# Optimization experiments

Measured on AMD Instinct MI355X. Metric: run time of the kernel, lower is better.

## Reference

```python
import jax, jax.numpy as jnp
import numpy as np

N_NODES = 50000
N_EDGES = 800000
HID = 64
N_LAYERS = 4
POS_DIM = 3
PARAM_SCALE = 0.1
POS_HEAD_SCALE = 0.001  # xavier gain=0.001 on final pos Linear


def setup_inputs() -> dict:
    key = jax.random.key(0)
    ks = jax.random.split(key, 12)
    L, H = N_LAYERS, HID
    s = PARAM_SCALE
    return {
        "x": jax.random.normal(ks[0], (N_NODES, HID), jnp.float32),
        "pos": jax.random.normal(ks[1], (N_NODES, POS_DIM), jnp.float32),
        "edge_index": jax.random.randint(ks[2], (2, N_EDGES), 0, N_NODES, jnp.int32),
        # edge MLP: Linear(2H+1 -> H), SiLU, Linear(H -> H), SiLU
        "We1": jax.random.normal(ks[3], (L, 2 * H + 1, H), jnp.float32) * s,
        "be1": jnp.zeros((L, H), jnp.float32),
        "We2": jax.random.normal(ks[4], (L, H, H), jnp.float32) * s,
        "be2": jnp.zeros((L, H), jnp.float32),
        # node MLP: Linear(2H -> H), SiLU, Linear(H -> H)
        "Wn1": jax.random.normal(ks[5], (L, 2 * H, H), jnp.float32) * s,
        "bn1": jnp.zeros((L, H), jnp.float32),
        "Wn2": jax.random.normal(ks[6], (L, H, H), jnp.float32) * s,
        "bn2": jnp.zeros((L, H), jnp.float32),
        # pos MLP: Linear(H -> H), SiLU, Linear(H -> 1) (tiny init)
        "Wp1": jax.random.normal(ks[7], (L, H, H), jnp.float32) * s,
        "bp1": jnp.zeros((L, H), jnp.float32),
        "Wp2": jax.random.normal(ks[8], (L, H, 1), jnp.float32) * POS_HEAD_SCALE,
        "bp2": jnp.zeros((L, 1), jnp.float32),
        # logit(pos_scale=0.5) == 0
        "pos_scale_logit": jnp.zeros((1,), jnp.float32),
    }


def reference(x, pos, edge_index, We1, be1, We2, be2, Wn1, bn1, Wn2, bn2,
              Wp1, bp1, Wp2, bp2, pos_scale_logit):
    POS_CLAMP = 500.0
    POS_UPDATE_CLAMP = 5.0
    src, dst = edge_index[0], edge_index[1]  # messages flow j=src -> i=dst
    n = x.shape[0]
    L = We1.shape[0]

    # pos is NOT fed back between layers in the torch forward, so edge
    # geometry is constant across layers.
    rel = pos[dst] - pos[src]                     # [E, P]
    d2 = jnp.sum(rel * rel, axis=-1, keepdims=True)  # [E, 1]
    deg = jnp.maximum(
        jax.ops.segment_sum(jnp.ones(src.shape, x.dtype), dst, num_segments=n),
        1.0)[:, None]                             # [N, 1]

    pos_new = pos
    for l in range(L):
        # edge MLP on gathered node pairs
        m = jnp.concatenate([x[dst], x[src], d2], axis=-1)  # [E, 2H+1]
        m = jax.nn.silu(m @ We1[l] + be1[l])
        m = jax.nn.silu(m @ We2[l] + be2[l])                # [E, H]
        # scatter-aggregate messages to target nodes
        agg = jax.ops.segment_sum(m, dst, num_segments=n)   # [N, H]
        # node update MLP
        h = jax.nn.silu(jnp.concatenate([x, agg], axis=-1) @ Wn1[l] + bn1[l])
        x = h @ Wn2[l] + bn2[l]
        # position update: mean over incoming edges of rel * phi_pos(m)
        c = jax.nn.silu(m @ Wp1[l] + bp1[l]) @ Wp2[l] + bp2[l]  # [E, 1]
        pos_new = pos + jax.ops.segment_sum(rel * c, dst, num_segments=n) / deg

    upd = (pos_new - pos) * jax.nn.sigmoid(pos_scale_logit[0])
    upd = jnp.clip(upd, -POS_UPDATE_CLAMP, POS_UPDATE_CLAMP)
    pos_out = jnp.clip(pos + upd, -POS_CLAMP, POS_CLAMP)
    return x, pos_out
```

## Files before the change

### kernel.cpp

```cpp
#include <hip/hip_runtime.h>

#define NN 50000
#define NE 800000
#define NTILES 12500
#define TPB 17

typedef __attribute__((ext_vector_type(8))) short short8;
typedef __attribute__((ext_vector_type(4))) float f32x4;

__device__ __forceinline__ float silu_f(float v) {
    return v / (1.0f + __expf(-v));
}
__device__ __forceinline__ unsigned short f2bf(float f) {
    unsigned u = __float_as_uint(f);
    u += 0x7fffu + ((u >> 16) & 1u);
    return (unsigned short)(u >> 16);
}
__device__ __forceinline__ unsigned pk2(float a, float b) {
    return (unsigned)f2bf(a) | ((unsigned)f2bf(b) << 16);
}
__device__ __forceinline__ void gload_lds16(const unsigned short* g, unsigned short* l) {
    __builtin_amdgcn_global_load_lds(
        (const __attribute__((address_space(1))) unsigned int*)g,
        (__attribute__((address_space(3))) unsigned int*)l, 16, 0, 0);
}
#define FENCE_BAR() do { \
    asm volatile("s_waitcnt lgkmcnt(0)" ::: "memory"); \
    __builtin_amdgcn_sched_barrier(0); \
    __builtin_amdgcn_s_barrier(); \
    __builtin_amdgcn_sched_barrier(0); \
} while (0)
#define VMDRAIN() do { \
    __builtin_amdgcn_sched_barrier(0); \
    asm volatile("s_waitcnt vmcnt(0)" ::: "memory"); \
    __builtin_amdgcn_sched_barrier(0); \
} while (0)

__global__ __launch_bounds__(256) void egnn_hist(
    const int* __restrict__ dst, int* __restrict__ hc)
{
    int e = blockIdx.x * 256 + threadIdx.x;
    if (e < NE) atomicAdd(&hc[dst[e]], 1);
}

__global__ __launch_bounds__(1024) void egnn_scan(
    int* __restrict__ hc, int* __restrict__ rowptr)
{
    __shared__ int part[1024];
    const int t = threadIdx.x;
    const int C = (NN + 1023) / 1024;
    const int b0 = t * C;
    int s = 0;
    for (int i = 0; i < C; ++i) {
        int idx = b0 + i;
        if (idx < NN) s += hc[idx];
    }
    part[t] = s;
    __syncthreads();
    for (int off = 1; off < 1024; off <<= 1) {
        int v = (t >= off) ? part[t - off] : 0;
        __syncthreads();
        part[t] += v;
        __syncthreads();
    }
    int run = part[t] - s;
    for (int i = 0; i < C; ++i) {
        int idx = b0 + i;
        if (idx < NN) {
            int v = hc[idx];
            rowptr[idx] = run;
            hc[idx] = run;
            run += v;
        }
    }
    if (t == 1023) rowptr[NN] = part[1023];
}

__global__ __launch_bounds__(256) void egnn_scatter(
    const int* __restrict__ src, const int* __restrict__ dst,
    const float* __restrict__ pos, int* __restrict__ cursor,
    int* __restrict__ eSrc, int* __restrict__ eDst, float* __restrict__ eD2)
{
    int e = blockIdx.x * 256 + threadIdx.x;
    if (e >= NE) return;
    int s = src[e], d = dst[e];
    float rx = pos[3*d+0] - pos[3*s+0];
    float ry = pos[3*d+1] - pos[3*s+1];
    float rz = pos[3*d+2] - pos[3*s+2];
    int p = atomicAdd(&cursor[d], 1);
    eSrc[p] = s;
    eDst[p] = d;
    eD2[p]  = rx*rx + ry*ry + rz*rz;
}

__global__ __launch_bounds__(256) void egnn_prep_w(
    const float* __restrict__ We1, const float* __restrict__ We2,
    unsigned short* __restrict__ Wg1, unsigned short* __restrict__ Wg2)
{
    int i = blockIdx.x * 256 + threadIdx.x;
    if (i < 4 * 64 * 128) {
        int k = i & 127, n = (i >> 7) & 63, l = i >> 13;
        Wg1[(size_t)(l * 64 + n) * 136 + k] = f2bf(We1[((size_t)l * 129 + k) * 64 + n]);
    }
    if (i < 4 * 64 * 64) {
        int h = i & 63, n = (i >> 6) & 63, l = i >> 12;
        Wg2[(size_t)(l * 64 + n) * 72 + h] = f2bf(We2[((size_t)l * 64 + h) * 64 + n]);
    }
}

__global__ __launch_bounds__(256) void egnn_prep_wn(
    const float* __restrict__ Wn1, const float* __restrict__ Wn2,
    unsigned short* __restrict__ Wgn1, unsigned short* __restrict__ Wgn2)
{
    int i = blockIdx.x * 256 + threadIdx.x;
    if (i < 4 * 64 * 128) {
        int k = i & 127, n = (i >> 7) & 63, l = i >> 13;
        Wgn1[(size_t)(l * 64 + n) * 136 + k] = f2bf(Wn1[((size_t)l * 128 + k) * 64 + n]);
    }
    if (i < 4 * 64 * 64) {
        int h = i & 63, n = (i >> 6) & 63, l = i >> 12;
        Wgn2[(size_t)(l * 64 + n) * 72 + h] = f2bf(Wn2[((size_t)l * 64 + h) * 64 + n]);
    }
}

__global__ __launch_bounds__(256) void egnn_xbf(
    const float* __restrict__ x, unsigned short* __restrict__ xbf)
{
    int i = blockIdx.x * 256 + threadIdx.x;
    if (i >= NN * 16) return;
    float4 v = ((const float4*)x)[i];
    ((uint2*)xbf)[i] = make_uint2(pk2(v.x, v.y), pk2(v.z, v.w));
}

template<bool POS>
__global__ __launch_bounds__(256) void egnn_edge(
    const unsigned short* __restrict__ xbf, const float* __restrict__ eD2,
    const int* __restrict__ eSrc, const int* __restrict__ eDst,
    const float* __restrict__ pos,
    const unsigned short* __restrict__ Wg1, const unsigned short* __restrict__ Wg2,
    const float* __restrict__ We1,
    const float* __restrict__ be1, const float* __restrict__ be2,
    const float* __restrict__ Wp1, const float* __restrict__ bp1,
    const float* __restrict__ Wp2, const float* __restrict__ bp2,
    float* __restrict__ agg, float* __restrict__ dpos, int layer)
{
    __shared__ __align__(16) unsigned char pool[16384 * 2 + 16640];
    __shared__ int   sS[2][64];
    __shared__ int   sD[2][64];
    __shared__ float s2[2][64];
    __shared__ float sC[64];

    unsigned short* const xls0 = (unsigned short*)pool;
    unsigned short* const xls1 = (unsigned short*)(pool + 16384);
    unsigned short* const m1l  = (unsigned short*)(pool + 32768);
    float* const          sM2f = (float*)(pool + 32768);

    const int t    = threadIdx.x;
    const int lane = t & 63;
    const int w    = t >> 6;
    const int l15  = lane & 15;
    const int g    = lane >> 4;
    const int eh   = w >> 1;
    const int ch   = w & 1;
    const int er   = lane >> 4;
    const int half = (lane >> 3) & 1;
    const int c    = lane & 7;
    const int tile0 = blockIdx.x * TPB;
    const int ntiles = (NTILES - tile0 < TPB) ? (NTILES - tile0) : TPB;

    const unsigned short* W1b = &Wg1[(size_t)(layer * 64) * 136];
    const unsigned short* W2b = &Wg2[(size_t)(layer * 64) * 72];
    short8 w1f0[4], w1f1[4], w2f0[2], w2f1[2];
    #pragma unroll
    for (int ks = 0; ks < 4; ++ks) {
        w1f0[ks] = *(const short8*)&W1b[(ch * 32 +      l15) * 136 + ks * 32 + g * 8];
        w1f1[ks] = *(const short8*)&W1b[(ch * 32 + 16 + l15) * 136 + ks * 32 + g * 8];
    }
    #pragma unroll
    for (int ks = 0; ks < 2; ++ks) {
        w2f0[ks] = *(const short8*)&W2b[(ch * 32 +      l15) * 72 + ks * 32 + g * 8];
        w2f1[ks] = *(const short8*)&W2b[(ch * 32 + 16 + l15) * 72 + ks * 32 + g * 8];
    }
    float4 wrv[2], b1v[2], b2v[2];
    {
        const float* Wr = &We1[((size_t)layer * 129 + 128) * 64];
        const float* B1 = &be1[layer * 64];
        const float* B2 = &be2[layer * 64];
        #pragma unroll
        for (int nt = 0; nt < 2; ++nt) {
            int n0 = ch * 32 + nt * 16 + g * 4;
            wrv[nt] = *(const float4*)&Wr[n0];
            b1v[nt] = *(const float4*)&B1[n0];
            b2v[nt] = *(const float4*)&B2[n0];
        }
    }

    const int* const ip = half ? eSrc : eDst;
    const int ebase = w * 16 + er;

    int nid[4];
    {
        const int gb0 = tile0 * 64;
        #pragma unroll
        for (int i = 0; i < 4; ++i) nid[i] = ip[gb0 + ebase + i * 4];
        #pragma unroll
        for (int i = 0; i < 4; ++i)
            gload_lds16(&xbf[(size_t)nid[i] * 64 + ((c ^ ((ebase + i * 4) & 7)) << 3)],
                        xls0 + w * 2048 + i * 512);
        __builtin_amdgcn_sched_barrier(0);
        if (ntiles > 1) {
            #pragma unroll
            for (int i = 0; i < 4; ++i) nid[i] = ip[gb0 + 64 + ebase + i * 4];
        }
        if (t < 64) { sS[0][t] = eSrc[gb0 + t]; sD[0][t] = eDst[gb0 + t]; s2[0][t] = eD2[gb0 + t]; }
    }
    int stS = 0, stD = 0; float st2 = 0.f;
    if (ntiles > 1 && t < 64) {
        const int gb1 = (tile0 + 1) * 64;
        stS = eSrc[gb1 + t]; stD = eDst[gb1 + t]; st2 = eD2[gb1 + t];
    }
    float bp2v = 0.f;
    if (POS) { bp2v = bp2[layer]; if (t < 64) sC[t] = bp2v; }
    VMDRAIN();
    FENCE_BAR();

    const f32x4 zero = {0.f, 0.f, 0.f, 0.f};

    for (int tt = 0; tt < ntiles; ++tt) {
        const int b = tt & 1;
        unsigned short* const xcur = b ? xls1 : xls0;
        unsigned short* const xnxt = b ? xls0 : xls1;

        if (tt + 1 < ntiles) {
            #pragma unroll
            for (int i = 0; i < 4; ++i)
                gload_lds16(&xbf[(size_t)nid[i] * 64 + ((c ^ ((ebase + i * 4) & 7)) << 3)],
                            xnxt + w * 2048 + i * 512);
            __builtin_amdgcn_sched_barrier(0);
            if (tt + 2 < ntiles) {
                const int gb2 = (tile0 + tt + 2) * 64;
                #pragma unroll
                for (int i = 0; i < 4; ++i) nid[i] = ip[gb2 + ebase + i * 4];
            }
        }

        f32x4 a00 = zero, a01 = zero, a10 = zero, a11 = zero;
        {
            const int r0 = (eh * 32 + l15) * 128;
            const int r1 = r0 + 16 * 128;
            const int r7 = l15 & 7;
            #pragma unroll
            for (int ks = 0; ks < 4; ++ks) {
                int col = (((ks << 2) + g) ^ r7) << 3;
                short8 fb0 = *(const short8*)&xcur[r0 + col];
                short8 fb1 = *(const short8*)&xcur[r1 + col];
                a00 = __builtin_amdgcn_mfma_f32_16x16x32_bf16(w1f0[ks], fb0, a00, 0, 0, 0);
                a01 = __builtin_amdgcn_mfma_f32_16x16x32_bf16(w1f0[ks], fb1, a01, 0, 0, 0);
                a10 = __builtin_amdgcn_mfma_f32_16x16x32_bf16(w1f1[ks], fb0, a10, 0, 0, 0);
                a11 = __builtin_amdgcn_mfma_f32_16x16x32_bf16(w1f1[ks], fb1, a11, 0, 0, 0);
            }
        }
        {
            float d2e0 = s2[b][eh * 32 + l15];
            float d2e1 = s2[b][eh * 32 + 16 + l15];
            int e0 = eh * 32 + l15;
            int e1 = e0 + 16;
            #pragma unroll
            for (int nt = 0; nt < 2; ++nt) {
                int n0 = ch * 32 + nt * 16 + g * 4;
                float4 wr = wrv[nt], bb = b1v[nt];
                f32x4 acc0 = nt ? a10 : a00;
                f32x4 acc1 = nt ? a11 : a01;
                float r0 = silu_f(acc0.x + d2e0 * wr.x + bb.x);
                float r1 = silu_f(acc0.y + d2e0 * wr.y + bb.y);
                float r2 = silu_f(acc0.z + d2e0 * wr.z + bb.z);
                float r3 = silu_f(acc0.w + d2e0 * wr.w + bb.w);
                *(uint2*)&m1l[e0 * 72 + n0] = make_uint2(pk2(r0, r1), pk2(r2, r3));
                r0 = silu_f(acc1.x + d2e1 * wr.x + bb.x);
                r1 = silu_f(acc1.y + d2e1 * wr.y + bb.y);
                r2 = silu_f(acc1.z + d2e1 * wr.z + bb.z);
                r3 = silu_f(acc1.w + d2e1 * wr.w + bb.w);
                *(uint2*)&m1l[e1 * 72 + n0] = make_uint2(pk2(r0, r1), pk2(r2, r3));
            }
        }
        FENCE_BAR();

        f32x4 c00 = zero, c01 = zero, c10 = zero, c11 = zero;
        #pragma unroll
        for (int ks = 0; ks < 2; ++ks) {
            short8 fb0 = *(const short8*)&m1l[(eh * 32 +      l15) * 72 + ks * 32 + g * 8];
            short8 fb1 = *(const short8*)&m1l[(eh * 32 + 16 + l15) * 72 + ks * 32 + g * 8];
            c00 = __builtin_amdgcn_mfma_f32_16x16x32_bf16(w2f0[ks], fb0, c00, 0, 0, 0);
            c01 = __builtin_amdgcn_mfma_f32_16x16x32_bf16(w2f0[ks], fb1, c01, 0, 0, 0);
            c10 = __builtin_amdgcn_mfma_f32_16x16x32_bf16(w2f1[ks], fb0, c10, 0, 0, 0);
            c11 = __builtin_amdgcn_mfma_f32_16x16x32_bf16(w2f1[ks], fb1, c11, 0, 0, 0);
        }
        FENCE_BAR();

        {
            int e0 = eh * 32 + l15;
            int e1 = e0 + 16;
            #pragma unroll
            for (int nt = 0; nt < 2; ++nt) {
                int n0 = ch * 32 + nt * 16 + g * 4;
                float4 bb = b2v[nt];
                f32x4 acc0 = nt ? c10 : c00;
                f32x4 acc1 = nt ? c11 : c01;
                sM2f[e0 * 65 + n0 + 0] = silu_f(acc0.x + bb.x);
                sM2f[e0 * 65 + n0 + 1] = silu_f(acc0.y + bb.y);
                sM2f[e0 * 65 + n0 + 2] = silu_f(acc0.z + bb.z);
                sM2f[e0 * 65 + n0 + 3] = silu_f(acc0.w + bb.w);
                sM2f[e1 * 65 + n0 + 0] = silu_f(acc1.x + bb.x);
                sM2f[e1 * 65 + n0 + 1] = silu_f(acc1.y + bb.y);
                sM2f[e1 * 65 + n0 + 2] = silu_f(acc1.z + bb.z);
                sM2f[e1 * 65 + n0 + 3] = silu_f(acc1.w + bb.w);
            }
        }
        if (tt + 1 < ntiles && t < 64) {
            sS[1 - b][t] = stS; sD[1 - b][t] = stD; s2[1 - b][t] = st2;
            if (tt + 2 < ntiles) {
                const int gb2 = (tile0 + tt + 2) * 64;
                stS = eSrc[gb2 + t]; stD = eDst[gb2 + t]; st2 = eD2[gb2 + t];
            }
        }
        FENCE_BAR();

        if (POS) {
            const int wofs = __builtin_amdgcn_readfirstlane(w * 16);
            float p1[16];
            {
                const float* bP1 = &bp1[(size_t)layer * 64 + wofs];
                #pragma unroll
                for (int hh = 0; hh < 16; ++hh) p1[hh] = bP1[hh];
            }
            const float* P1 = &Wp1[(size_t)layer * 64 * 64 + wofs];
            for (int k = 0; k < 64; ++k) {
                float mv = sM2f[lane * 65 + k];
                const float* wr2 = P1 + k * 64;
                #pragma unroll
                for (int hh = 0; hh < 16; ++hh) p1[hh] = fmaf(mv, wr2[hh], p1[hh]);
            }
            float part = 0.0f;
            {
                const float* P2 = &Wp2[(size_t)layer * 64 + wofs];
                #pragma unroll
                for (int hh = 0; hh < 16; ++hh) part += silu_f(p1[hh]) * P2[hh];
            }
            atomicAdd(&sC[lane], part);
            FENCE_BAR();
            if (w == 0) {
                float cc = sC[lane];
                int d = sD[b][lane], s = sS[b][lane];
                float rx = pos[3*d+0] - pos[3*s+0];
                float ry = pos[3*d+1] - pos[3*s+1];
                float rz = pos[3*d+2] - pos[3*s+2];
                atomicAdd(&dpos[3*(size_t)d+0], rx * cc);
                atomicAdd(&dpos[3*(size_t)d+1], ry * cc);
                atomicAdd(&dpos[3*(size_t)d+2], rz * cc);
            }
            FENCE_BAR();
            if (t < 64) sC[t] = bp2v;
        }

        VMDRAIN();

        {
            const int e0 = w * 16;
            float v[16];
            #pragma unroll
            for (int i = 0; i < 16; ++i) v[i] = sM2f[(e0 + i) * 65 + lane];
            int dd[16];
            #pragma unroll
            for (int i = 0; i < 16; ++i) dd[i] = sD[b][e0 + i];
            float run = v[0];
            int cur = dd[0];
            #pragma unroll
            for (int i = 1; i < 16; ++i) {
                if (dd[i] != cur) {
                    atomicAdd(&agg[(size_t)cur * 64 + lane], run);
                    run = 0.0f;
                    cur = dd[i];
                }
                run += v[i];
            }
            atomicAdd(&agg[(size_t)cur * 64 + lane], run);
        }
        FENCE_BAR();
    }
}

template<bool WRITE_F32>
__global__ __launch_bounds__(256) void egnn_node_mfma(
    const unsigned short* __restrict__ xbf, const float* __restrict__ agg,
    const unsigned short* __restrict__ Wgn1, const unsigned short* __restrict__ Wgn2,
    const float* __restrict__ bn1, const float* __restrict__ bn2,
    float* __restrict__ xout, unsigned short* __restrict__ xbf_out, int layer)
{
    __shared__ __align__(16) unsigned char pool[16384 + 9216];
    unsigned short* const xpl = (unsigned short*)pool;
    unsigned short* const m1l = (unsigned short*)(pool + 16384);
    float* const          sXf = (float*)pool;

    const int t    = threadIdx.x;
    const int lane = t & 63;
    const int w    = t >> 6;
    const int l15  = lane & 15;
    const int g    = lane >> 4;
    const int eh   = w >> 1;
    const int ch   = w & 1;
    const int base = blockIdx.x * 64;
    const int nval = (NN - base < 64) ? (NN - base) : 64;

    #pragma unroll
    for (int i = 0; i < 2; ++i) {
        int e = w * 16 + i * 8 + (lane >> 3);
        int node = base + ((e < nval) ? e : 0);
        gload_lds16(&xbf[(size_t)node * 64 + (((lane & 7) ^ (e & 7)) << 3)],
                    xpl + w * 1024 + i * 512);
    }
    __builtin_amdgcn_sched_barrier(0);

    const unsigned short* W1b = &Wgn1[(size_t)(layer * 64) * 136];
    const unsigned short* W2b = &Wgn2[(size_t)(layer * 64) * 72];
    short8 w1f0[4], w1f1[4], w2f0[2], w2f1[2];
    #pragma unroll
    for (int ks = 0; ks < 4; ++ks) {
        w1f0[ks] = *(const short8*)&W1b[(ch * 32 +      l15) * 136 + ks * 32 + g * 8];
        w1f1[ks] = *(const short8*)&W1b[(ch * 32 + 16 + l15) * 136 + ks * 32 + g * 8];
    }
    #pragma unroll
    for (int ks = 0; ks < 2; ++ks) {
        w2f0[ks] = *(const short8*)&W2b[(ch * 32 +      l15) * 72 + ks * 32 + g * 8];
        w2f1[ks] = *(const short8*)&W2b[(ch * 32 + 16 + l15) * 72 + ks * 32 + g * 8];
    }
    float4 b1v[2], b2v[2];
    {
        const float* B1 = &bn1[layer * 64];
        const float* B2 = &bn2[layer * 64];
        #pragma unroll
        for (int nt = 0; nt < 2; ++nt) {
            int n0 = ch * 32 + nt * 16 + g * 4;
            b1v[nt] = *(const float4*)&B1[n0];
            b2v[nt] = *(const float4*)&B2[n0];
        }
    }

    {
        int e = t >> 2, q = t & 3;
        int node = base + ((e < nval) ? e : 0);
        const float4* ap = (const float4*)&agg[(size_t)node * 64 + q * 16];
        float4 v0 = ap[0], v1 = ap[1], v2 = ap[2], v3 = ap[3];
        uint4 u0, u1;
        u0.x = pk2(v0.x, v0.y); u0.y = pk2(v0.z, v0.w);
        u0.z = pk2(v1.x, v1.y); u0.w = pk2(v1.z, v1.w);
        u1.x = pk2(v2.x, v2.y); u1.y = pk2(v2.z, v2.w);
        u1.z = pk2(v3.x, v3.y); u1.w = pk2(v3.z, v3.w);
        *(uint4*)&xpl[4096 + e * 64 + (((2 * q)     ^ (e & 7)) << 3)] = u0;
        *(uint4*)&xpl[4096 + e * 64 + (((2 * q + 1) ^ (e & 7)) << 3)] = u1;
    }
    __syncthreads();

    const f32x4 zero = {0.f, 0.f, 0.f, 0.f};
    f32x4 a00 = zero, a01 = zero, a10 = zero, a11 = zero;
    {
        const int e0 = eh * 32 + l15;
        const int e1 = e0 + 16;
        const int r7 = e0 & 7;
        #pragma unroll
        for (int ks = 0; ks < 4; ++ks) {
            int kc = (ks << 2) + g;
            int off0 = (kc >> 3) * 4096 + e0 * 64 + (((kc & 7) ^ r7) << 3);
            int off1 = (kc >> 3) * 4096 + e1 * 64 + (((kc & 7) ^ r7) << 3);
            short8 fb0 = *(const short8*)&xpl[off0];
            short8 fb1 = *(const short8*)&xpl[off1];
            a00 = __builtin_amdgcn_mfma_f32_16x16x32_bf16(w1f0[ks], fb0, a00, 0, 0, 0);
            a01 = __builtin_amdgcn_mfma_f32_16x16x32_bf16(w1f0[ks], fb1, a01, 0, 0, 0);
            a10 = __builtin_amdgcn_mfma_f32_16x16x32_bf16(w1f1[ks], fb0, a10, 0, 0, 0);
            a11 = __builtin_amdgcn_mfma_f32_16x16x32_bf16(w1f1[ks], fb1, a11, 0, 0, 0);
        }
    }
    {
        int e0 = eh * 32 + l15;
        int e1 = e0 + 16;
        #pragma unroll
        for (int nt = 0; nt < 2; ++nt) {
            int n0 = ch * 32 + nt * 16 + g * 4;
            float4 bb = b1v[nt];
            f32x4 acc0 = nt ? a10 : a00;
            f32x4 acc1 = nt ? a11 : a01;
            float r0 = silu_f(acc0.x + bb.x);
            float r1 = silu_f(acc0.y + bb.y);
            float r2 = silu_f(acc0.z + bb.z);
            float r3 = silu_f(acc0.w + bb.w);
            *(uint2*)&m1l[e0 * 72 + n0] = make_uint2(pk2(r0, r1), pk2(r2, r3));
            r0 = silu_f(acc1.x + bb.x);
            r1 = silu_f(acc1.y + bb.y);
            r2 = silu_f(acc1.z + bb.z);
            r3 = silu_f(acc1.w + bb.w);
            *(uint2*)&m1l[e1 * 72 + n0] = make_uint2(pk2(r0, r1), pk2(r2, r3));
        }
    }
    __syncthreads();

    f32x4 c00 = zero, c01 = zero, c10 = zero, c11 = zero;
    #pragma unroll
    for (int ks = 0; ks < 2; ++ks) {
        short8 fb0 = *(const short8*)&m1l[(eh * 32 +      l15) * 72 + ks * 32 + g * 8];
        short8 fb1 = *(const short8*)&m1l[(eh * 32 + 16 + l15) * 72 + ks * 32 + g * 8];
        c00 = __builtin_amdgcn_mfma_f32_16x16x32_bf16(w2f0[ks], fb0, c00, 0, 0, 0);
        c01 = __builtin_amdgcn_mfma_f32_16x16x32_bf16(w2f0[ks], fb1, c01, 0, 0, 0);
        c10 = __builtin_amdgcn_mfma_f32_16x16x32_bf16(w2f1[ks], fb0, c10, 0, 0, 0);
        c11 = __builtin_amdgcn_mfma_f32_16x16x32_bf16(w2f1[ks], fb1, c11, 0, 0, 0);
    }
    __syncthreads();

    {
        int e0 = eh * 32 + l15;
        int e1 = e0 + 16;
        #pragma unroll
        for (int nt = 0; nt < 2; ++nt) {
            int n0 = ch * 32 + nt * 16 + g * 4;
            float4 bb = b2v[nt];
            f32x4 acc0 = nt ? c10 : c00;
            f32x4 acc1 = nt ? c11 : c01;
            sXf[e0 * 65 + n0 + 0] = acc0.x + bb.x;
            sXf[e0 * 65 + n0 + 1] = acc0.y + bb.y;
            sXf[e0 * 65 + n0 + 2] = acc0.z + bb.z;
            sXf[e0 * 65 + n0 + 3] = acc0.w + bb.w;
            sXf[e1 * 65 + n0 + 0] = acc1.x + bb.x;
            sXf[e1 * 65 + n0 + 1] = acc1.y + bb.y;
            sXf[e1 * 65 + n0 + 2] = acc1.z + bb.z;
            sXf[e1 * 65 + n0 + 3] = acc1.w + bb.w;
        }
    }
    __syncthreads();

    if (WRITE_F32) {
        #pragma unroll
        for (int i = 0; i < 4; ++i) {
            int idx = i * 256 + t;
            int e = idx >> 4, c = idx & 15;
            if (e < nval) {
                float4 v;
                const float* p = &sXf[e * 65 + c * 4];
                v.x = p[0]; v.y = p[1]; v.z = p[2]; v.w = p[3];
                *reinterpret_cast<float4*>(&xout[(size_t)(base + e) * 64 + c * 4]) = v;
            }
        }
    }
    {
        int e = t >> 2, q = t & 3;
        if (e < nval) {
            const float* p = &sXf[e * 65 + q * 16];
            uint4 u0, u1;
            u0.x = pk2(p[0],  p[1]);  u0.y = pk2(p[2],  p[3]);
            u0.z = pk2(p[4],  p[5]);  u0.w = pk2(p[6],  p[7]);
            u1.x = pk2(p[8],  p[9]);  u1.y = pk2(p[10], p[11]);
            u1.z = pk2(p[12], p[13]); u1.w = pk2(p[14], p[15]);
            *(uint4*)&xbf_out[(size_t)(base + e) * 64 + q * 16 + 0] = u0;
            *(uint4*)&xbf_out[(size_t)(base + e) * 64 + q * 16 + 8] = u1;
        }
    }
}

__global__ __launch_bounds__(256) void egnn_final(
    const float* __restrict__ pos, const float* __restrict__ dpos,
    const int* __restrict__ rowptr, const float* __restrict__ logit,
    float* __restrict__ pos_out)
{
    int i = blockIdx.x * 256 + threadIdx.x;
    if (i >= NN * 3) return;
    int node = i / 3;
    float dg = fmaxf((float)(rowptr[node + 1] - rowptr[node]), 1.0f);
    float sig = 1.0f / (1.0f + __expf(-logit[0]));
    float upd = (dpos[i] / dg) * sig;
    upd = fminf(fmaxf(upd, -5.0f), 5.0f);
    float p = pos[i] + upd;
    pos_out[i] = fminf(fmaxf(p, -500.0f), 500.0f);
}

extern "C" void kernel_launch(void* const* d_in, const int* in_sizes, int n_in,
                              void* d_out, int out_size, void* d_ws, size_t ws_size,
                              hipStream_t stream)
{
    const float* x0    = (const float*)d_in[0];
    const float* pos   = (const float*)d_in[1];
    const int*   src   = (const int*)d_in[2];
    const int*   dst   = src + NE;
    const float* We1   = (const float*)d_in[3];
    const float* be1   = (const float*)d_in[4];
    const float* We2   = (const float*)d_in[5];
    const float* be2   = (const float*)d_in[6];
    const float* Wn1   = (const float*)d_in[7];
    const float* bn1   = (const float*)d_in[8];
    const float* Wn2   = (const float*)d_in[9];
    const float* bn2   = (const float*)d_in[10];
    const float* Wp1   = (const float*)d_in[11];
    const float* bp1   = (const float*)d_in[12];
    const float* Wp2   = (const float*)d_in[13];
    const float* bp2   = (const float*)d_in[14];
    const float* logit = (const float*)d_in[15];

    float* xout    = (float*)d_out;
    float* pos_out = xout + (size_t)NN * 64;

    float* ws  = (float*)d_ws;
    float* agg  = ws;  ws += (size_t)NN * 64;
    float* dpos = ws;  ws += (size_t)NN * 3;
    float* eD2  = ws;  ws += NE;
    int* rowptr = (int*)ws;  ws += NN + 1;
    int* hc     = (int*)ws;  ws += NN;
    int* eSrc   = (int*)ws;  ws += NE;
    int* eDst   = (int*)ws;  ws += NE;
    unsigned short* xbf = (unsigned short*)ws;
    ws += (size_t)NN * 32;
    unsigned short* Wg1  = (unsigned short*)ws;
    unsigned short* Wg2  = Wg1 + 4 * 64 * 136;
    unsigned short* Wgn1 = Wg2 + 4 * 64 * 72;
    unsigned short* Wgn2 = Wgn1 + 4 * 64 * 136;

    hipMemsetAsync(hc, 0, NN * sizeof(int), stream);
    hipMemsetAsync(dpos, 0, (size_t)NN * 3 * sizeof(float), stream);
    egnn_hist<<<NE / 256, 256, 0, stream>>>(dst, hc);
    egnn_scan<<<1, 1024, 0, stream>>>(hc, rowptr);
    egnn_scatter<<<NE / 256, 256, 0, stream>>>(src, dst, pos, hc, eSrc, eDst, eD2);
    egnn_prep_w<<<128, 256, 0, stream>>>(We1, We2, Wg1, Wg2);
    egnn_prep_wn<<<128, 256, 0, stream>>>(Wn1, Wn2, Wgn1, Wgn2);
    egnn_xbf<<<(NN * 16 + 255) / 256, 256, 0, stream>>>(x0, xbf);

    const int nblk = (NTILES + TPB - 1) / TPB;
    const int nodeblk = (NN + 63) / 64;
    for (int l = 0; l < 4; ++l) {
        hipMemsetAsync(agg, 0, (size_t)NN * 64 * sizeof(float), stream);
        if (l == 3) {
            egnn_edge<true><<<nblk, 256, 0, stream>>>(
                xbf, eD2, eSrc, eDst, pos, Wg1, Wg2, We1, be1, be2,
                Wp1, bp1, Wp2, bp2, agg, dpos, l);
            egnn_node_mfma<true><<<nodeblk, 256, 0, stream>>>(
                xbf, agg, Wgn1, Wgn2, bn1, bn2, xout, xbf, l);
        } else {
            egnn_edge<false><<<nblk, 256, 0, stream>>>(
                xbf, eD2, eSrc, eDst, pos, Wg1, Wg2, We1, be1, be2,
                Wp1, bp1, Wp2, bp2, agg, dpos, l);
            egnn_node_mfma<false><<<nodeblk, 256, 0, stream>>>(
                xbf, agg, Wgn1, Wgn2, bn1, bn2, xout, xbf, l);
        }
    }
    egnn_final<<<(NN * 3 + 255) / 256, 256, 0, stream>>>(pos, dpos, rowptr, logit, pos_out);
}
```

Before: 991.2 us.

## Make edge kernel wave-independent, move pos MLP to MFMA, drop block barriers

The edge kernel now has each wavefront own its 16 edges end to end. Each wave holds the full 64-wide weights in registers and uses private LDS buffers for m1 and m2, which removes the block-wide barriers between the edge-MLP stages. The position MLP's first linear layer becomes a bf16 MFMA with pre-converted weights instead of a scalar FMA loop, and m2 is kept in bf16 for both the aggregation and the pos MLP. TPB drops to 10 and launch bounds request 3 blocks per CU; the extra weight registers could limit occupancy, and the pos path adds bf16 rounding.

```diff
diff --git a/kernel.cpp b/kernel.cpp
--- a/kernel.cpp
+++ b/kernel.cpp
@@ -3,7 +3,7 @@
 #define NN 50000
 #define NE 800000
 #define NTILES 12500
-#define TPB 17
+#define TPB 10
 
 typedef __attribute__((ext_vector_type(8))) short short8;
 typedef __attribute__((ext_vector_type(4))) float f32x4;
@@ -19,17 +19,14 @@
 __device__ __forceinline__ unsigned pk2(float a, float b) {
     return (unsigned)f2bf(a) | ((unsigned)f2bf(b) << 16);
 }
+__device__ __forceinline__ float bf2f(unsigned short v) {
+    return __uint_as_float((unsigned)v << 16);
+}
 __device__ __forceinline__ void gload_lds16(const unsigned short* g, unsigned short* l) {
     __builtin_amdgcn_global_load_lds(
         (const __attribute__((address_space(1))) unsigned int*)g,
         (__attribute__((address_space(3))) unsigned int*)l, 16, 0, 0);
 }
-#define FENCE_BAR() do { \
-    asm volatile("s_waitcnt lgkmcnt(0)" ::: "memory"); \
-    __builtin_amdgcn_sched_barrier(0); \
-    __builtin_amdgcn_s_barrier(); \
-    __builtin_amdgcn_sched_barrier(0); \
-} while (0)
 #define VMDRAIN() do { \
     __builtin_amdgcn_sched_barrier(0); \
     asm volatile("s_waitcnt vmcnt(0)" ::: "memory"); \
@@ -95,7 +92,9 @@
 
 __global__ __launch_bounds__(256) void egnn_prep_w(
     const float* __restrict__ We1, const float* __restrict__ We2,
-    unsigned short* __restrict__ Wg1, unsigned short* __restrict__ Wg2)
+    const float* __restrict__ Wp1,
+    unsigned short* __restrict__ Wg1, unsigned short* __restrict__ Wg2,
+    unsigned short* __restrict__ Wgp1)
 {
     int i = blockIdx.x * 256 + threadIdx.x;
     if (i < 4 * 64 * 128) {
@@ -104,7 +103,8 @@
     }
     if (i < 4 * 64 * 64) {
         int h = i & 63, n = (i >> 6) & 63, l = i >> 12;
-        Wg2[(size_t)(l * 64 + n) * 72 + h] = f2bf(We2[((size_t)l * 64 + h) * 64 + n]);
+        Wg2[(size_t)(l * 64 + n) * 72 + h]  = f2bf(We2[((size_t)l * 64 + h) * 64 + n]);
+        Wgp1[(size_t)(l * 64 + n) * 72 + h] = f2bf(Wp1[((size_t)l * 64 + h) * 64 + n]);
     }
 }
 
@@ -133,67 +133,39 @@
 }
 
 template<bool POS>
-__global__ __launch_bounds__(256) void egnn_edge(
+__global__ __launch_bounds__(256, 3) void egnn_edge(
     const unsigned short* __restrict__ xbf, const float* __restrict__ eD2,
     const int* __restrict__ eSrc, const int* __restrict__ eDst,
     const float* __restrict__ pos,
     const unsigned short* __restrict__ Wg1, const unsigned short* __restrict__ Wg2,
+    const unsigned short* __restrict__ Wgp1,
     const float* __restrict__ We1,
     const float* __restrict__ be1, const float* __restrict__ be2,
-    const float* __restrict__ Wp1, const float* __restrict__ bp1,
-    const float* __restrict__ Wp2, const float* __restrict__ bp2,
+    const float* __restrict__ bp1, const float* __restrict__ Wp2,
+    const float* __restrict__ bp2,
     float* __restrict__ agg, float* __restrict__ dpos, int layer)
 {
-    __shared__ __align__(16) unsigned char pool[16384 * 2 + 16640];
-    __shared__ int   sS[2][64];
-    __shared__ int   sD[2][64];
-    __shared__ float s2[2][64];
-    __shared__ float sC[64];
-
-    unsigned short* const xls0 = (unsigned short*)pool;
-    unsigned short* const xls1 = (unsigned short*)(pool + 16384);
-    unsigned short* const m1l  = (unsigned short*)(pool + 32768);
-    float* const          sM2f = (float*)(pool + 32768);
+    __shared__ __align__(16) unsigned short xls[2][4][2048];
+    __shared__ __align__(16) unsigned short m1s[4][1152];
+    __shared__ __align__(16) unsigned short m2s[4][1152];
+    __shared__ float sBias[192];
 
     const int t    = threadIdx.x;
     const int lane = t & 63;
     const int w    = t >> 6;
     const int l15  = lane & 15;
     const int g    = lane >> 4;
-    const int eh   = w >> 1;
-    const int ch   = w & 1;
+    const int g4   = g * 4;
     const int er   = lane >> 4;
     const int half = (lane >> 3) & 1;
     const int c    = lane & 7;
     const int tile0 = blockIdx.x * TPB;
     const int ntiles = (NTILES - tile0 < TPB) ? (NTILES - tile0) : TPB;
 
-    const unsigned short* W1b = &Wg1[(size_t)(layer * 64) * 136];
-    const unsigned short* W2b = &Wg2[(size_t)(layer * 64) * 72];
-    short8 w1f0[4], w1f1[4], w2f0[2], w2f1[2];
-    #pragma unroll
-    for (int ks = 0; ks < 4; ++ks) {
-        w1f0[ks] = *(const short8*)&W1b[(ch * 32 +      l15) * 136 + ks * 32 + g * 8];
-        w1f1[ks] = *(const short8*)&W1b[(ch * 32 + 16 + l15) * 136 + ks * 32 + g * 8];
-    }
-    #pragma unroll
-    for (int ks = 0; ks < 2; ++ks) {
-        w2f0[ks] = *(const short8*)&W2b[(ch * 32 +      l15) * 72 + ks * 32 + g * 8];
-        w2f1[ks] = *(const short8*)&W2b[(ch * 32 + 16 + l15) * 72 + ks * 32 + g * 8];
-    }
-    float4 wrv[2], b1v[2], b2v[2];
-    {
-        const float* Wr = &We1[((size_t)layer * 129 + 128) * 64];
-        const float* B1 = &be1[layer * 64];
-        const float* B2 = &be2[layer * 64];
-        #pragma unroll
-        for (int nt = 0; nt < 2; ++nt) {
-            int n0 = ch * 32 + nt * 16 + g * 4;
-            wrv[nt] = *(const float4*)&Wr[n0];
-            b1v[nt] = *(const float4*)&B1[n0];
-            b2v[nt] = *(const float4*)&B2[n0];
-        }
-    }
+    unsigned short* const xw0 = &xls[0][w][0];
+    unsigned short* const xw1 = &xls[1][w][0];
+    unsigned short* const m1w = &m1s[w][0];
+    unsigned short* const m2w = &m2s[w][0];
 
     const int* const ip = half ? eSrc : eDst;
     const int ebase = w * 16 + er;
@@ -206,36 +178,49 @@
         #pragma unroll
         for (int i = 0; i < 4; ++i)
             gload_lds16(&xbf[(size_t)nid[i] * 64 + ((c ^ ((ebase + i * 4) & 7)) << 3)],
-                        xls0 + w * 2048 + i * 512);
+                        xw0 + i * 512);
         __builtin_amdgcn_sched_barrier(0);
         if (ntiles > 1) {
             #pragma unroll
             for (int i = 0; i < 4; ++i) nid[i] = ip[gb0 + 64 + ebase + i * 4];
         }
-        if (t < 64) { sS[0][t] = eSrc[gb0 + t]; sD[0][t] = eDst[gb0 + t]; s2[0][t] = eD2[gb0 + t]; }
-    }
-    int stS = 0, stD = 0; float st2 = 0.f;
-    if (ntiles > 1 && t < 64) {
-        const int gb1 = (tile0 + 1) * 64;
-        stS = eSrc[gb1 + t]; stD = eDst[gb1 + t]; st2 = eD2[gb1 + t];
-    }
-    float bp2v = 0.f;
-    if (POS) { bp2v = bp2[layer]; if (t < 64) sC[t] = bp2v; }
-    VMDRAIN();
-    FENCE_BAR();
+    }
+    short8 w1f[4][4], w2f[2][4];
+    {
+        const unsigned short* W1b = &Wg1[(size_t)(layer * 64) * 136];
+        const unsigned short* W2b = &Wg2[(size_t)(layer * 64) * 72];
+        #pragma unroll
+        for (int ks = 0; ks < 4; ++ks)
+            #pragma unroll
+            for (int m = 0; m < 4; ++m)
+                w1f[ks][m] = *(const short8*)&W1b[(size_t)(m * 16 + l15) * 136 + ks * 32 + g * 8];
+        #pragma unroll
+        for (int ks = 0; ks < 2; ++ks)
+            #pragma unroll
+            for (int m = 0; m < 4; ++m)
+                w2f[ks][m] = *(const short8*)&W2b[(size_t)(m * 16 + l15) * 72 + ks * 32 + g * 8];
+    }
+    if (t < 64) {
+        sBias[t]       = We1[((size_t)layer * 129 + 128) * 64 + t];
+        sBias[64 + t]  = be1[(size_t)layer * 64 + t];
+        sBias[128 + t] = be2[(size_t)layer * 64 + t];
+    }
+    __syncthreads();
 
     const f32x4 zero = {0.f, 0.f, 0.f, 0.f};
 
     for (int tt = 0; tt < ntiles; ++tt) {
-        const int b = tt & 1;
-        unsigned short* const xcur = b ? xls1 : xls0;
-        unsigned short* const xnxt = b ? xls0 : xls1;
+        const int gb = (tile0 + tt) * 64;
+        unsigned short* const xcur = (tt & 1) ? xw1 : xw0;
+        unsigned short* const xnxt = (tt & 1) ? xw0 : xw1;
+
+        VMDRAIN();
 
         if (tt + 1 < ntiles) {
             #pragma unroll
             for (int i = 0; i < 4; ++i)
                 gload_lds16(&xbf[(size_t)nid[i] * 64 + ((c ^ ((ebase + i * 4) & 7)) << 3)],
-                            xnxt + w * 2048 + i * 512);
+                            xnxt + i * 512);
             __builtin_amdgcn_sched_barrier(0);
             if (tt + 2 < ntiles) {
                 const int gb2 = (tile0 + tt + 2) * 64;
@@ -244,148 +229,101 @@
             }
         }
 
-        f32x4 a00 = zero, a01 = zero, a10 = zero, a11 = zero;
+        const float d2e = eD2[gb + w * 16 + l15];
+
+        f32x4 a[4] = {zero, zero, zero, zero};
         {
-            const int r0 = (eh * 32 + l15) * 128;
-            const int r1 = r0 + 16 * 128;
             const int r7 = l15 & 7;
             #pragma unroll
             for (int ks = 0; ks < 4; ++ks) {
-                int col = (((ks << 2) + g) ^ r7) << 3;
-                short8 fb0 = *(const short8*)&xcur[r0 + col];
-                short8 fb1 = *(const short8*)&xcur[r1 + col];
-                a00 = __builtin_amdgcn_mfma_f32_16x16x32_bf16(w1f0[ks], fb0, a00, 0, 0, 0);
-                a01 = __builtin_amdgcn_mfma_f32_16x16x32_bf16(w1f0[ks], fb1, a01, 0, 0, 0);
-                a10 = __builtin_amdgcn_mfma_f32_16x16x32_bf16(w1f1[ks], fb0, a10, 0, 0, 0);
-                a11 = __builtin_amdgcn_mfma_f32_16x16x32_bf16(w1f1[ks], fb1, a11, 0, 0, 0);
-            }
-        }
-        {
-            float d2e0 = s2[b][eh * 32 + l15];
-            float d2e1 = s2[b][eh * 32 + 16 + l15];
-            int e0 = eh * 32 + l15;
-            int e1 = e0 + 16;
-            #pragma unroll
-            for (int nt = 0; nt < 2; ++nt) {
-                int n0 = ch * 32 + nt * 16 + g * 4;
-                float4 wr = wrv[nt], bb = b1v[nt];
-                f32x4 acc0 = nt ? a10 : a00;
-                f32x4 acc1 = nt ? a11 : a01;
-                float r0 = silu_f(acc0.x + d2e0 * wr.x + bb.x);
-                float r1 = silu_f(acc0.y + d2e0 * wr.y + bb.y);
-                float r2 = silu_f(acc0.z + d2e0 * wr.z + bb.z);
-                float r3 = silu_f(acc0.w + d2e0 * wr.w + bb.w);
-                *(uint2*)&m1l[e0 * 72 + n0] = make_uint2(pk2(r0, r1), pk2(r2, r3));
-                r0 = silu_f(acc1.x + d2e1 * wr.x + bb.x);
-                r1 = silu_f(acc1.y + d2e1 * wr.y + bb.y);
-                r2 = silu_f(acc1.z + d2e1 * wr.z + bb.z);
-                r3 = silu_f(acc1.w + d2e1 * wr.w + bb.w);
-                *(uint2*)&m1l[e1 * 72 + n0] = make_uint2(pk2(r0, r1), pk2(r2, r3));
-            }
-        }
-        FENCE_BAR();
-
-        f32x4 c00 = zero, c01 = zero, c10 = zero, c11 = zero;
+                short8 fb = *(const short8*)&xcur[l15 * 128 + ((((ks << 2) + g) ^ r7) << 3)];
+                #pragma unroll
+                for (int m = 0; m < 4; ++m)
+                    a[m] = __builtin_amdgcn_mfma_f32_16x16x32_bf16(w1f[ks][m], fb, a[m], 0, 0, 0);
+            }
+        }
+        #pragma unroll
+        for (int m = 0; m < 4; ++m) {
+            float4 wr = *(const float4*)&sBias[m * 16 + g4];
+            float4 bb = *(const float4*)&sBias[64 + m * 16 + g4];
+            float r0 = silu_f(a[m].x + d2e * wr.x + bb.x);
+            float r1 = silu_f(a[m].y + d2e * wr.y + bb.y);
+            float r2 = silu_f(a[m].z + d2e * wr.z + bb.z);
+            float r3 = silu_f(a[m].w + d2e * wr.w + bb.w);
+            *(uint2*)&m1w[l15 * 72 + m * 16 + g4] = make_uint2(pk2(r0, r1), pk2(r2, r3));
+        }
+
+        f32x4 cc[4] = {zero, zero, zero, zero};
         #pragma unroll
         for (int ks = 0; ks < 2; ++ks) {
-            short8 fb0 = *(const short8*)&m1l[(eh * 32 +      l15) * 72 + ks * 32 + g * 8];
-            short8 fb1 = *(const short8*)&m1l[(eh * 32 + 16 + l15) * 72 + ks * 32 + g * 8];
-            c00 = __builtin_amdgcn_mfma_f32_16x16x32_bf16(w2f0[ks], fb0, c00, 0, 0, 0);
-            c01 = __builtin_amdgcn_mfma_f32_16x16x32_bf16(w2f0[ks], fb1, c01, 0, 0, 0);
-            c10 = __builtin_amdgcn_mfma_f32_16x16x32_bf16(w2f1[ks], fb0, c10, 0, 0, 0);
-            c11 = __builtin_amdgcn_mfma_f32_16x16x32_bf16(w2f1[ks], fb1, c11, 0, 0, 0);
-        }
-        FENCE_BAR();
-
-        {
-            int e0 = eh * 32 + l15;
-            int e1 = e0 + 16;
-            #pragma unroll
-            for (int nt = 0; nt < 2; ++nt) {
-                int n0 = ch * 32 + nt * 16 + g * 4;
-                float4 bb = b2v[nt];
-                f32x4 acc0 = nt ? c10 : c00;
-                f32x4 acc1 = nt ? c11 : c01;
-                sM2f[e0 * 65 + n0 + 0] = silu_f(acc0.x + bb.x);
-                sM2f[e0 * 65 + n0 + 1] = silu_f(acc0.y + bb.y);
-                sM2f[e0 * 65 + n0 + 2] = silu_f(acc0.z + bb.z);
-                sM2f[e0 * 65 + n0 + 3] = silu_f(acc0.w + bb.w);
-                sM2f[e1 * 65 + n0 + 0] = silu_f(acc1.x + bb.x);
-                sM2f[e1 * 65 + n0 + 1] = silu_f(acc1.y + bb.y);
-                sM2f[e1 * 65 + n0 + 2] = silu_f(acc1.z + bb.z);
-                sM2f[e1 * 65 + n0 + 3] = silu_f(acc1.w + bb.w);
-            }
-        }
-        if (tt + 1 < ntiles && t < 64) {
-            sS[1 - b][t] = stS; sD[1 - b][t] = stD; s2[1 - b][t] = st2;
-            if (tt + 2 < ntiles) {
-                const int gb2 = (tile0 + tt + 2) * 64;
-                stS = eSrc[gb2 + t]; stD = eDst[gb2 + t]; st2 = eD2[gb2 + t];
-            }
-        }
-        FENCE_BAR();
+            short8 fb = *(const short8*)&m1w[l15 * 72 + ks * 32 + g * 8];
+            #pragma unroll
+            for (int m = 0; m < 4; ++m)
+                cc[m] = __builtin_amdgcn_mfma_f32_16x16x32_bf16(w2f[ks][m], fb, cc[m], 0, 0, 0);
+        }
+        #pragma unroll
+        for (int m = 0; m < 4; ++m) {
+            float4 bb = *(const float4*)&sBias[128 + m * 16 + g4];
+            float r0 = silu_f(cc[m].x + bb.x);
+            float r1 = silu_f(cc[m].y + bb.y);
+            float r2 = silu_f(cc[m].z + bb.z);
+            float r3 = silu_f(cc[m].w + bb.w);
+            *(uint2*)&m2w[l15 * 72 + m * 16 + g4] = make_uint2(pk2(r0, r1), pk2(r2, r3));
+        }
 
         if (POS) {
-            const int wofs = __builtin_amdgcn_readfirstlane(w * 16);
-            float p1[16];
-            {
-                const float* bP1 = &bp1[(size_t)layer * 64 + wofs];
+            f32x4 pa[4] = {zero, zero, zero, zero};
+            const unsigned short* WPb = &Wgp1[(size_t)(layer * 64) * 72];
+            #pragma unroll
+            for (int ks = 0; ks < 2; ++ks) {
+                short8 fb = *(const short8*)&m2w[l15 * 72 + ks * 32 + g * 8];
                 #pragma unroll
-                for (int hh = 0; hh < 16; ++hh) p1[hh] = bP1[hh];
-            }
-            const float* P1 = &Wp1[(size_t)layer * 64 * 64 + wofs];
-            for (int k = 0; k < 64; ++k) {
-                float mv = sM2f[lane * 65 + k];
-                const float* wr2 = P1 + k * 64;
-                #pragma unroll
-                for (int hh = 0; hh < 16; ++hh) p1[hh] = fmaf(mv, wr2[hh], p1[hh]);
+                for (int m = 0; m < 4; ++m) {
+                    short8 wf = *(const short8*)&WPb[(size_t)(m * 16 + l15) * 72 + ks * 32 + g * 8];
+                    pa[m] = __builtin_amdgcn_mfma_f32_16x16x32_bf16(wf, fb, pa[m], 0, 0, 0);
+                }
             }
             float part = 0.0f;
-            {
-                const float* P2 = &Wp2[(size_t)layer * 64 + wofs];
-                #pragma unroll
-                for (int hh = 0; hh < 16; ++hh) part += silu_f(p1[hh]) * P2[hh];
-            }
-            atomicAdd(&sC[lane], part);
-            FENCE_BAR();
-            if (w == 0) {
-                float cc = sC[lane];
-                int d = sD[b][lane], s = sS[b][lane];
+            #pragma unroll
+            for (int m = 0; m < 4; ++m) {
+                float4 b1 = *(const float4*)&bp1[(size_t)layer * 64 + m * 16 + g4];
+                float4 w2 = *(const float4*)&Wp2[(size_t)layer * 64 + m * 16 + g4];
+                part += silu_f(pa[m].x + b1.x) * w2.x;
+                part += silu_f(pa[m].y + b1.y) * w2.y;
+                part += silu_f(pa[m].z + b1.z) * w2.z;
+                part += silu_f(pa[m].w + b1.w) * w2.w;
+            }
+            part += __shfl_xor(part, 16);
+            part += __shfl_xor(part, 32);
+            if (lane < 16) {
+                float cv = part + bp2[layer];
+                int ge = gb + w * 16 + lane;
+                int d = eDst[ge], s = eSrc[ge];
                 float rx = pos[3*d+0] - pos[3*s+0];
                 float ry = pos[3*d+1] - pos[3*s+1];
                 float rz = pos[3*d+2] - pos[3*s+2];
-                atomicAdd(&dpos[3*(size_t)d+0], rx * cc);
-                atomicAdd(&dpos[3*(size_t)d+1], ry * cc);
-                atomicAdd(&dpos[3*(size_t)d+2], rz * cc);
-            }
-            FENCE_BAR();
-            if (t < 64) sC[t] = bp2v;
-        }
-
-        VMDRAIN();
+                atomicAdd(&dpos[3*(size_t)d+0], rx * cv);
+                atomicAdd(&dpos[3*(size_t)d+1], ry * cv);
+                atomicAdd(&dpos[3*(size_t)d+2], rz * cv);
+            }
+        }
 
         {
-            const int e0 = w * 16;
-            float v[16];
-            #pragma unroll
-            for (int i = 0; i < 16; ++i) v[i] = sM2f[(e0 + i) * 65 + lane];
-            int dd[16];
-            #pragma unroll
-            for (int i = 0; i < 16; ++i) dd[i] = sD[b][e0 + i];
-            float run = v[0];
-            int cur = dd[0];
-            #pragma unroll
-            for (int i = 1; i < 16; ++i) {
-                if (dd[i] != cur) {
+            float run = 0.0f;
+            int cur = eDst[gb + w * 16];
+            #pragma unroll
+            for (int i = 0; i < 16; ++i) {
+                int d = eDst[gb + w * 16 + i];
+                float v = bf2f(m2w[i * 72 + lane]);
+                if (i > 0 && d != cur) {
                     atomicAdd(&agg[(size_t)cur * 64 + lane], run);
                     run = 0.0f;
-                    cur = dd[i];
                 }
-                run += v[i];
+                cur = d;
+                run += v;
             }
             atomicAdd(&agg[(size_t)cur * 64 + lane], run);
         }
-        FENCE_BAR();
     }
 }
 
@@ -618,13 +556,14 @@
     unsigned short* Wg2  = Wg1 + 4 * 64 * 136;
     unsigned short* Wgn1 = Wg2 + 4 * 64 * 72;
     unsigned short* Wgn2 = Wgn1 + 4 * 64 * 136;
+    unsigned short* Wgp1 = Wgn2 + 4 * 64 * 72;
 
     hipMemsetAsync(hc, 0, NN * sizeof(int), stream);
     hipMemsetAsync(dpos, 0, (size_t)NN * 3 * sizeof(float), stream);
     egnn_hist<<<NE / 256, 256, 0, stream>>>(dst, hc);
     egnn_scan<<<1, 1024, 0, stream>>>(hc, rowptr);
     egnn_scatter<<<NE / 256, 256, 0, stream>>>(src, dst, pos, hc, eSrc, eDst, eD2);
-    egnn_prep_w<<<128, 256, 0, stream>>>(We1, We2, Wg1, Wg2);
+    egnn_prep_w<<<128, 256, 0, stream>>>(We1, We2, Wp1, Wg1, Wg2, Wgp1);
     egnn_prep_wn<<<128, 256, 0, stream>>>(Wn1, Wn2, Wgn1, Wgn2);
     egnn_xbf<<<(NN * 16 + 255) / 256, 256, 0, stream>>>(x0, xbf);
 
@@ -634,14 +573,14 @@
         hipMemsetAsync(agg, 0, (size_t)NN * 64 * sizeof(float), stream);
         if (l == 3) {
             egnn_edge<true><<<nblk, 256, 0, stream>>>(
-                xbf, eD2, eSrc, eDst, pos, Wg1, Wg2, We1, be1, be2,
-                Wp1, bp1, Wp2, bp2, agg, dpos, l);
+                xbf, eD2, eSrc, eDst, pos, Wg1, Wg2, Wgp1, We1, be1, be2,
+                bp1, Wp2, bp2, agg, dpos, l);
             egnn_node_mfma<true><<<nodeblk, 256, 0, stream>>>(
                 xbf, agg, Wgn1, Wgn2, bn1, bn2, xout, xbf, l);
         } else {
             egnn_edge<false><<<nblk, 256, 0, stream>>>(
-                xbf, eD2, eSrc, eDst, pos, Wg1, Wg2, We1, be1, be2,
-                Wp1, bp1, Wp2, bp2, agg, dpos, l);
+                xbf, eD2, eSrc, eDst, pos, Wg1, Wg2, Wgp1, We1, be1, be2,
+                bp1, Wp2, bp2, agg, dpos, l);
             egnn_node_mfma<false><<<nodeblk, 256, 0, stream>>>(
                 xbf, agg, Wgn1, Wgn2, bn1, bn2, xout, xbf, l);
         }
```

New measurement: 998.2 us. Within noise of the previous version (+0.7%).
